# Optimization experiments

Hardware: AMD Instinct MI355X
Metric: run time of the kernel (lower is better)

Reference implementation:

```python
import jax, jax.numpy as jnp
import numpy as np

N_NODES = 50000
N_EDGES = 800000
D = 128


def setup_inputs() -> dict:
    key = jax.random.key(0)
    ks = jax.random.split(key, 6)
    stdv = 1.0 / np.sqrt(D)
    inputs = {
        "input": jax.random.normal(ks[0], (N_NODES, D), dtype=jnp.float32),
        "h0": jax.random.normal(ks[1], (N_NODES, D), dtype=jnp.float32),
        # COO representation of the (normalized) sparse adjacency
        "vals": jax.random.uniform(ks[2], (N_EDGES,), dtype=jnp.float32) / 16.0,
        "weight": jax.random.uniform(ks[3], (D, D), dtype=jnp.float32, minval=-stdv, maxval=stdv),
        "lamda": jnp.float32(0.5),
        "alpha": jnp.float32(0.1),
        "row": jax.random.randint(ks[4], (N_EDGES,), 0, N_NODES),
        "col": jax.random.randint(ks[5], (N_EDGES,), 0, N_NODES),
        "l": 4,
    }
    return inputs


def reference(input, h0, vals, weight, lamda, alpha, row, col, l):
    # theta = log(lamda / l + 1)
    theta = jnp.log(lamda / l + 1.0)
    # hi = spmm(adj, input): gather source-node features, scale by edge
    # values, scatter-add into destination rows.  [E, D] -> [N, D]
    hi = jax.ops.segment_sum(vals[:, None] * input[col], row, num_segments=input.shape[0])
    # variant=False path
    support = (1.0 - alpha) * hi + alpha * h0
    r = support
    # output = theta * support @ W + (1 - theta) * r
    output = theta * jnp.matmul(support, weight) + (1.0 - theta) * r
    return output
```

## Files before the change

kernel.cpp:

```cpp
#include <hip/hip_runtime.h>
#include <cmath>

constexpr int N_NODES = 50000;
constexpr int N_EDGES = 800000;
constexpr int D = 128;
constexpr int BM = 128;
constexpr int CAP = 32;
constexpr int OVF_CAP = 8192;

constexpr int NPART = 8;
constexpr int ROWS_PER_PART = (N_NODES + NPART - 1) / NPART;
constexpr int EPB = 8192;
constexpr int BPP = (N_EDGES + EPB - 1) / EPB;

constexpr int PRE_BLOCKS  = (N_EDGES / 4 + 255) / 256;
constexpr int CAST_BLOCKS = (N_NODES * D / 8 + 255) / 256;

constexpr size_t OFF_OVFCNT = 200000;
constexpr size_t OFF_BUCKET = 200064;
constexpr size_t OFF_OVF    = 6600064;
constexpr size_t OFF_PACKED = 6731136;
constexpr size_t OFF_ECV    = 19531136;
constexpr size_t OFF_ROW16  = 22731136;

__device__ __forceinline__ unsigned bf16rn(float f) {
    unsigned u = __float_as_uint(f);
    return (u + 0x7fffu + ((u >> 16) & 1u)) >> 16;
}
__device__ __forceinline__ float bf_lo(unsigned u) { return __uint_as_float(u << 16); }
__device__ __forceinline__ float bf_hi(unsigned u) { return __uint_as_float(u & 0xffff0000u); }

__device__ __forceinline__ unsigned enc_val(float v) {
    int m = (int)(v * 1048576.0f + 0.5f);
    if (m > 65535) m = 65535;
    if (m < 0) m = 0;
    return (unsigned)m;
}

__global__ __launch_bounds__(256) void prepack_cast(
    const int* __restrict__ row, const int* __restrict__ col,
    const float* __restrict__ vals, const float* __restrict__ input,
    ushort* __restrict__ row16, unsigned* __restrict__ ecv,
    unsigned* __restrict__ packed)
{
    if (blockIdx.x < PRE_BLOCKS) {
        int i = blockIdx.x * 256 + threadIdx.x;
        if (i >= N_EDGES / 4) return;
        int4   r4 = ((const int4*)row)[i];
        int4   c4 = ((const int4*)col)[i];
        float4 v4 = ((const float4*)vals)[i];
        ushort4 r16;
        r16.x = (unsigned short)r4.x; r16.y = (unsigned short)r4.y;
        r16.z = (unsigned short)r4.z; r16.w = (unsigned short)r4.w;
        uint4 e4;
        e4.x = (unsigned)c4.x | (enc_val(v4.x) << 16);
        e4.y = (unsigned)c4.y | (enc_val(v4.y) << 16);
        e4.z = (unsigned)c4.z | (enc_val(v4.z) << 16);
        e4.w = (unsigned)c4.w | (enc_val(v4.w) << 16);
        ((ushort4*)row16)[i] = r16;
        ((uint4*)ecv)[i] = e4;
    } else {
        int i = (blockIdx.x - PRE_BLOCKS) * 256 + threadIdx.x;
        if (i >= N_NODES * D / 8) return;
        const float4* f = (const float4*)(input + (size_t)i * 8);
        float4 a = f[0], b = f[1];
        uint4 o;
        o.x = bf16rn(a.x) | (bf16rn(a.y) << 16);
        o.y = bf16rn(a.z) | (bf16rn(a.w) << 16);
        o.z = bf16rn(b.x) | (bf16rn(b.y) << 16);
        o.w = bf16rn(b.z) | (bf16rn(b.w) << 16);
        ((uint4*)packed)[i] = o;
    }
}

__global__ __launch_bounds__(256) void part_scatter(
    const ushort* __restrict__ row16, const unsigned* __restrict__ ecv,
    int* __restrict__ cnt, unsigned* __restrict__ bucket,
    int* __restrict__ ovf_cnt, int4* __restrict__ ovf)
{
    const int p  = blockIdx.x & (NPART - 1);
    const int cb = blockIdx.x / NPART;
    const int lo = p * ROWS_PER_PART;
    const int hi = lo + ROWS_PER_PART;
    const int gbase = cb * (EPB / 4);

    #pragma unroll
    for (int it = 0; it < EPB / 4 / 256; ++it) {
        int gi = gbase + it * 256 + threadIdx.x;
        if (gi >= N_EDGES / 4) break;
        ushort4 r4 = ((const ushort4*)row16)[gi];
        int e = gi * 4;
        int r;
        r = r4.x;
        if (r >= lo && r < hi) {
            unsigned ent = ecv[e];
            int pos = atomicAdd(&cnt[r], 1);
            if (pos < CAP) bucket[(size_t)r * CAP + pos] = ent;
            else { int o = atomicAdd(ovf_cnt, 1);
                   if (o < OVF_CAP) ovf[o] = make_int4(r, (int)(ent & 0xffffu),
                       __float_as_int((float)(ent >> 16) * (1.0f / 1048576.0f)), 0); }
        }
        r = r4.y;
        if (r >= lo && r < hi) {
            unsigned ent = ecv[e + 1];
            int pos = atomicAdd(&cnt[r], 1);
            if (pos < CAP) bucket[(size_t)r * CAP + pos] = ent;
            else { int o = atomicAdd(ovf_cnt, 1);
                   if (o < OVF_CAP) ovf[o] = make_int4(r, (int)(ent & 0xffffu),
                       __float_as_int((float)(ent >> 16) * (1.0f / 1048576.0f)), 0); }
        }
        r = r4.z;
        if (r >= lo && r < hi) {
            unsigned ent = ecv[e + 2];
            int pos = atomicAdd(&cnt[r], 1);
            if (pos < CAP) bucket[(size_t)r * CAP + pos] = ent;
            else { int o = atomicAdd(ovf_cnt, 1);
                   if (o < OVF_CAP) ovf[o] = make_int4(r, (int)(ent & 0xffffu),
                       __float_as_int((float)(ent >> 16) * (1.0f / 1048576.0f)), 0); }
        }
        r = r4.w;
        if (r >= lo && r < hi) {
            unsigned ent = ecv[e + 3];
            int pos = atomicAdd(&cnt[r], 1);
            if (pos < CAP) bucket[(size_t)r * CAP + pos] = ent;
            else { int o = atomicAdd(ovf_cnt, 1);
                   if (o < OVF_CAP) ovf[o] = make_int4(r, (int)(ent & 0xffffu),
                       __float_as_int((float)(ent >> 16) * (1.0f / 1048576.0f)), 0); }
        }
    }
}

__global__ __launch_bounds__(256) void gather_support(
    const unsigned* __restrict__ packed,
    const float* __restrict__ h0,
    const float* __restrict__ alpha_p,
    const int* __restrict__ cnt,
    const unsigned* __restrict__ bucket,
    float* __restrict__ support)
{
    const float alpha = *alpha_p;
    const float oma = 1.0f - alpha;
    const int wv   = threadIdx.x >> 6;
    const int lane = threadIdx.x & 63;
    const int q    = lane & 15;
    const int half = lane >> 4;

    const int g = blockIdx.x * 4 + wv;
    if (g >= N_NODES) return;

    int n = cnt[g];
    if (n > CAP) n = CAP;
    const unsigned* b = bucket + (size_t)g * CAP;
    const uint4* pk = (const uint4*)packed;

    float acc[8] = {0.f, 0.f, 0.f, 0.f, 0.f, 0.f, 0.f, 0.f};
    int e = half;
    for (; e + 4 < n; e += 8) {
        unsigned m0 = b[e];
        unsigned m1 = b[e + 4];
        float v0 = (float)(m0 >> 16) * (1.0f / 1048576.0f);
        float v1 = (float)(m1 >> 16) * (1.0f / 1048576.0f);
        uint4 x0 = pk[(size_t)(m0 & 0xffffu) * 16 + q];
        uint4 x1 = pk[(size_t)(m1 & 0xffffu) * 16 + q];
        acc[0] += v0 * bf_lo(x0.x); acc[1] += v0 * bf_hi(x0.x);
        acc[2] += v0 * bf_lo(x0.y); acc[3] += v0 * bf_hi(x0.y);
        acc[4] += v0 * bf_lo(x0.z); acc[5] += v0 * bf_hi(x0.z);
        acc[6] += v0 * bf_lo(x0.w); acc[7] += v0 * bf_hi(x0.w);
        acc[0] += v1 * bf_lo(x1.x); acc[1] += v1 * bf_hi(x1.x);
        acc[2] += v1 * bf_lo(x1.y); acc[3] += v1 * bf_hi(x1.y);
        acc[4] += v1 * bf_lo(x1.z); acc[5] += v1 * bf_hi(x1.z);
        acc[6] += v1 * bf_lo(x1.w); acc[7] += v1 * bf_hi(x1.w);
    }
    if (e < n) {
        unsigned m = b[e];
        float v = (float)(m >> 16) * (1.0f / 1048576.0f);
        uint4 x = pk[(size_t)(m & 0xffffu) * 16 + q];
        acc[0] += v * bf_lo(x.x); acc[1] += v * bf_hi(x.x);
        acc[2] += v * bf_lo(x.y); acc[3] += v * bf_hi(x.y);
        acc[4] += v * bf_lo(x.z); acc[5] += v * bf_hi(x.z);
        acc[6] += v * bf_lo(x.w); acc[7] += v * bf_hi(x.w);
    }
    #pragma unroll
    for (int j = 0; j < 8; ++j) {
        acc[j] += __shfl_xor(acc[j], 16);
        acc[j] += __shfl_xor(acc[j], 32);
    }
    if (half == 0) {
        const float* hp = h0 + (size_t)g * D + q * 8;
        float4 ha = *(const float4*)(hp);
        float4 hb = *(const float4*)(hp + 4);
        float* sp = support + (size_t)g * D + q * 8;
        float4 sa, sb;
        sa.x = oma * acc[0] + alpha * ha.x;
        sa.y = oma * acc[1] + alpha * ha.y;
        sa.z = oma * acc[2] + alpha * ha.z;
        sa.w = oma * acc[3] + alpha * ha.w;
        sb.x = oma * acc[4] + alpha * hb.x;
        sb.y = oma * acc[5] + alpha * hb.y;
        sb.z = oma * acc[6] + alpha * hb.z;
        sb.w = oma * acc[7] + alpha * hb.w;
        *(float4*)(sp) = sa;
        *(float4*)(sp + 4) = sb;
    }
}

__global__ __launch_bounds__(256) void ovf_apply(
    const float* __restrict__ input,
    const float* __restrict__ alpha_p,
    const int* __restrict__ ovf_cnt,
    const int4* __restrict__ ovf,
    float* __restrict__ support)
{
    int n = *ovf_cnt;
    if (n > OVF_CAP) n = OVF_CAP;
    const float oma = 1.0f - *alpha_p;
    for (int i = blockIdx.x * 256 + threadIdx.x; i < n * 2; i += gridDim.x * 256) {
        int idx = i >> 1, part = i & 1;
        int4 m = ovf[idx];
        float v = oma * __int_as_float(m.z);
        const float* x = input + (size_t)m.y * D + part * 64;
        float* s = support + (size_t)m.x * D + part * 64;
        for (int k = 0; k < 64; ++k) atomicAdd(&s[k], v * x[k]);
    }
}

__global__ __launch_bounds__(512, 1) void gemm_inplace(
    const float* __restrict__ weight,
    const float* __restrict__ lamda_p,
    const int* __restrict__ l_p,
    float* __restrict__ data)
{
    __shared__ float sW[D * D];
    __shared__ float sS[BM * (D + 4)];

    const int tid = threadIdx.x;
    const float lamda = *lamda_p;
    const float theta = logf(lamda / (float)(*l_p) + 1.0f);
    const float omt = 1.0f - theta;

    {
        const float4* W4 = (const float4*)weight;
        float4* sW4 = (float4*)sW;
        #pragma unroll
        for (int i = 0; i < 8; ++i)
            sW4[tid + i * 512] = W4[tid + i * 512];
    }

    const int row0 = blockIdx.x * BM;
    #pragma unroll
    for (int ii = 0; ii < 8; ++ii) {
        int i = tid + ii * 512;
        int rr = i >> 5;
        int cc = (i & 31) << 2;
        int g = row0 + rr;
        float4 s = make_float4(0.f, 0.f, 0.f, 0.f);
        if (g < N_NODES) s = *(const float4*)(data + (size_t)g * D + cc);
        *(float4*)(sS + rr * (D + 4) + cc) = s;
    }
    __syncthreads();

    const int tx = tid & 31;
    const int ty = tid >> 5;
    const int jc = tx << 2;
    const int rbase = ty << 3;

    float acc[8][4] = {};
    for (int k = 0; k < D; k += 4) {
        float4 w0 = *(const float4*)(sW + (k + 0) * D + jc);
        float4 w1 = *(const float4*)(sW + (k + 1) * D + jc);
        float4 w2 = *(const float4*)(sW + (k + 2) * D + jc);
        float4 w3 = *(const float4*)(sW + (k + 3) * D + jc);
        #pragma unroll
        for (int i = 0; i < 8; ++i) {
            float4 s = *(const float4*)(sS + (rbase + i) * (D + 4) + k);
            acc[i][0] += s.x * w0.x + s.y * w1.x + s.z * w2.x + s.w * w3.x;
            acc[i][1] += s.x * w0.y + s.y * w1.y + s.z * w2.y + s.w * w3.y;
            acc[i][2] += s.x * w0.z + s.y * w1.z + s.z * w2.z + s.w * w3.z;
            acc[i][3] += s.x * w0.w + s.y * w1.w + s.z * w2.w + s.w * w3.w;
        }
    }

    #pragma unroll
    for (int i = 0; i < 8; ++i) {
        int g = row0 + rbase + i;
        if (g >= N_NODES) continue;
        float4 s = *(const float4*)(sS + (rbase + i) * (D + 4) + jc);
        float4 o;
        o.x = theta * acc[i][0] + omt * s.x;
        o.y = theta * acc[i][1] + omt * s.y;
        o.z = theta * acc[i][2] + omt * s.z;
        o.w = theta * acc[i][3] + omt * s.w;
        *(float4*)(data + (size_t)g * D + jc) = o;
    }
}

extern "C" void kernel_launch(void* const* d_in, const int* in_sizes, int n_in,
                              void* d_out, int out_size, void* d_ws, size_t ws_size,
                              hipStream_t stream) {
    const float* input  = (const float*)d_in[0];
    const float* h0     = (const float*)d_in[1];
    const float* vals   = (const float*)d_in[2];
    const float* weight = (const float*)d_in[3];
    const float* lamda  = (const float*)d_in[4];
    const float* alpha  = (const float*)d_in[5];
    const int*   row    = (const int*)d_in[6];
    const int*   col    = (const int*)d_in[7];
    const int*   l      = (const int*)d_in[8];
    float* out = (float*)d_out;

    char* ws = (char*)d_ws;
    int*      cnt     = (int*)ws;
    int*      ovf_cnt = (int*)(ws + OFF_OVFCNT);
    unsigned* bucket  = (unsigned*)(ws + OFF_BUCKET);
    int4*     ovf     = (int4*)(ws + OFF_OVF);
    unsigned* packed  = (unsigned*)(ws + OFF_PACKED);
    unsigned* ecv     = (unsigned*)(ws + OFF_ECV);
    ushort*   row16   = (ushort*)(ws + OFF_ROW16);

    hipMemsetAsync(ws, 0, OFF_BUCKET, stream);

    prepack_cast<<<PRE_BLOCKS + CAST_BLOCKS, 256, 0, stream>>>(
        row, col, vals, input, row16, ecv, packed);

    part_scatter<<<NPART * BPP, 256, 0, stream>>>(
        row16, ecv, cnt, bucket, ovf_cnt, ovf);

    int gatherb = (N_NODES + 3) / 4;
    gather_support<<<gatherb, 256, 0, stream>>>(packed, h0, alpha, cnt, bucket, out);

    ovf_apply<<<8, 256, 0, stream>>>(input, alpha, ovf_cnt, ovf, out);

    int gemmb = (N_NODES + BM - 1) / BM;
    gemm_inplace<<<gemmb, 512, 0, stream>>>(weight, lamda, l, out);
}
```

Measured before the change: 229.1 us.

## Replace FP32 FMA GEMM with bf16 MFMA GEMM using pre-transposed weight

The dense support@W stage moves from a scalar FP32 shared-memory GEMM to a 16x16x32 bf16 MFMA kernel. Support rows are cast to bf16 while being staged into LDS. An extra block in the prepack kernel converts and transposes the weight to bf16 once. The aim is to cut the ALU cost of the 50000x128x128 GEMM and raise occupancy with smaller 64-row tiles. In exchange, the matmul inputs lose precision to bf16 and the epilogue writes are column-strided per lane rather than float4-vectorized.

```diff
diff --git a/kernel.cpp b/kernel.cpp
--- a/kernel.cpp
+++ b/kernel.cpp
@@ -4,7 +4,6 @@
 constexpr int N_NODES = 50000;
 constexpr int N_EDGES = 800000;
 constexpr int D = 128;
-constexpr int BM = 128;
 constexpr int CAP = 32;
 constexpr int OVF_CAP = 8192;
 
@@ -22,6 +21,10 @@
 constexpr size_t OFF_PACKED = 6731136;
 constexpr size_t OFF_ECV    = 19531136;
 constexpr size_t OFF_ROW16  = 22731136;
+constexpr size_t OFF_WT     = 24331136;
+
+typedef __attribute__((ext_vector_type(8))) short bf16x8;
+typedef __attribute__((ext_vector_type(4))) float f32x4;
 
 __device__ __forceinline__ unsigned bf16rn(float f) {
     unsigned u = __float_as_uint(f);
@@ -40,8 +43,9 @@
 __global__ __launch_bounds__(256) void prepack_cast(
     const int* __restrict__ row, const int* __restrict__ col,
     const float* __restrict__ vals, const float* __restrict__ input,
+    const float* __restrict__ weight,
     ushort* __restrict__ row16, unsigned* __restrict__ ecv,
-    unsigned* __restrict__ packed)
+    unsigned* __restrict__ packed, ushort* __restrict__ wt)
 {
     if (blockIdx.x < PRE_BLOCKS) {
         int i = blockIdx.x * 256 + threadIdx.x;
@@ -59,7 +63,7 @@
         e4.w = (unsigned)c4.w | (enc_val(v4.w) << 16);
         ((ushort4*)row16)[i] = r16;
         ((uint4*)ecv)[i] = e4;
-    } else {
+    } else if (blockIdx.x < PRE_BLOCKS + CAST_BLOCKS) {
         int i = (blockIdx.x - PRE_BLOCKS) * 256 + threadIdx.x;
         if (i >= N_NODES * D / 8) return;
         const float4* f = (const float4*)(input + (size_t)i * 8);
@@ -70,6 +74,13 @@
         o.z = bf16rn(b.x) | (bf16rn(b.y) << 16);
         o.w = bf16rn(b.z) | (bf16rn(b.w) << 16);
         ((uint4*)packed)[i] = o;
+    } else {
+        #pragma unroll
+        for (int j = 0; j < 64; ++j) {
+            int idx = threadIdx.x + j * 256;
+            int k = idx >> 7, n = idx & 127;
+            wt[n * 128 + k] = (ushort)bf16rn(weight[idx]);
+        }
     }
 }
 
@@ -224,73 +235,74 @@
     }
 }
 
-__global__ __launch_bounds__(512, 1) void gemm_inplace(
-    const float* __restrict__ weight,
+__global__ __launch_bounds__(256) void gemm_mfma(
+    const ushort* __restrict__ wt,
     const float* __restrict__ lamda_p,
     const int* __restrict__ l_p,
     float* __restrict__ data)
 {
-    __shared__ float sW[D * D];
-    __shared__ float sS[BM * (D + 4)];
+    constexpr int SP = 136;
+    __shared__ ushort sA[64 * SP];
+    __shared__ ushort sB[128 * SP];
 
     const int tid = threadIdx.x;
     const float lamda = *lamda_p;
     const float theta = logf(lamda / (float)(*l_p) + 1.0f);
     const float omt = 1.0f - theta;
-
-    {
-        const float4* W4 = (const float4*)weight;
-        float4* sW4 = (float4*)sW;
-        #pragma unroll
-        for (int i = 0; i < 8; ++i)
-            sW4[tid + i * 512] = W4[tid + i * 512];
-    }
-
-    const int row0 = blockIdx.x * BM;
-    #pragma unroll
-    for (int ii = 0; ii < 8; ++ii) {
-        int i = tid + ii * 512;
-        int rr = i >> 5;
-        int cc = (i & 31) << 2;
+    const int row0 = blockIdx.x * 64;
+
+    #pragma unroll
+    for (int j = 0; j < 8; ++j) {
+        int idx = j * 256 + tid;
+        int n  = idx >> 4;
+        int k8 = (idx & 15) << 3;
+        *(uint4*)(&sB[n * SP + k8]) = ((const uint4*)wt)[idx];
+    }
+    #pragma unroll
+    for (int j = 0; j < 8; ++j) {
+        int idx = j * 256 + tid;
+        int rr = idx >> 5;
+        int c4 = (idx & 31) << 2;
         int g = row0 + rr;
         float4 s = make_float4(0.f, 0.f, 0.f, 0.f);
-        if (g < N_NODES) s = *(const float4*)(data + (size_t)g * D + cc);
-        *(float4*)(sS + rr * (D + 4) + cc) = s;
+        if (g < N_NODES) s = *(const float4*)(data + (size_t)g * D + c4);
+        uint2 pkv;
+        pkv.x = bf16rn(s.x) | (bf16rn(s.y) << 16);
+        pkv.y = bf16rn(s.z) | (bf16rn(s.w) << 16);
+        *(uint2*)(&sA[rr * SP + c4]) = pkv;
     }
     __syncthreads();
 
-    const int tx = tid & 31;
-    const int ty = tid >> 5;
-    const int jc = tx << 2;
-    const int rbase = ty << 3;
-
-    float acc[8][4] = {};
-    for (int k = 0; k < D; k += 4) {
-        float4 w0 = *(const float4*)(sW + (k + 0) * D + jc);
-        float4 w1 = *(const float4*)(sW + (k + 1) * D + jc);
-        float4 w2 = *(const float4*)(sW + (k + 2) * D + jc);
-        float4 w3 = *(const float4*)(sW + (k + 3) * D + jc);
+    const int wave = tid >> 6;
+    const int lane = tid & 63;
+    const int m    = lane & 15;
+    const int quad = lane >> 4;
+    const int arow = wave * 16 + m;
+
+    f32x4 acc[8] = {};
+    #pragma unroll
+    for (int kb = 0; kb < 4; ++kb) {
+        bf16x8 a = *(const bf16x8*)(&sA[arow * SP + kb * 32 + quad * 8]);
         #pragma unroll
-        for (int i = 0; i < 8; ++i) {
-            float4 s = *(const float4*)(sS + (rbase + i) * (D + 4) + k);
-            acc[i][0] += s.x * w0.x + s.y * w1.x + s.z * w2.x + s.w * w3.x;
-            acc[i][1] += s.x * w0.y + s.y * w1.y + s.z * w2.y + s.w * w3.y;
-            acc[i][2] += s.x * w0.z + s.y * w1.z + s.z * w2.z + s.w * w3.z;
-            acc[i][3] += s.x * w0.w + s.y * w1.w + s.z * w2.w + s.w * w3.w;
-        }
-    }
-
-    #pragma unroll
-    for (int i = 0; i < 8; ++i) {
-        int g = row0 + rbase + i;
-        if (g >= N_NODES) continue;
-        float4 s = *(const float4*)(sS + (rbase + i) * (D + 4) + jc);
-        float4 o;
-        o.x = theta * acc[i][0] + omt * s.x;
-        o.y = theta * acc[i][1] + omt * s.y;
-        o.z = theta * acc[i][2] + omt * s.z;
-        o.w = theta * acc[i][3] + omt * s.w;
-        *(float4*)(data + (size_t)g * D + jc) = o;
+        for (int nt = 0; nt < 8; ++nt) {
+            bf16x8 b = *(const bf16x8*)(&sB[(nt * 16 + m) * SP + kb * 32 + quad * 8]);
+            acc[nt] = __builtin_amdgcn_mfma_f32_16x16x32_bf16(a, b, acc[nt], 0, 0, 0);
+        }
+    }
+
+    const int gbase = row0 + wave * 16 + quad * 4;
+    #pragma unroll
+    for (int nt = 0; nt < 8; ++nt) {
+        int colb = nt * 16 + m;
+        #pragma unroll
+        for (int i = 0; i < 4; ++i) {
+            int g = gbase + i;
+            if (g < N_NODES) {
+                size_t off = (size_t)g * D + colb;
+                float s = data[off];
+                data[off] = theta * acc[nt][i] + omt * s;
+            }
+        }
     }
 }
 
@@ -316,11 +328,12 @@
     unsigned* packed  = (unsigned*)(ws + OFF_PACKED);
     unsigned* ecv     = (unsigned*)(ws + OFF_ECV);
     ushort*   row16   = (ushort*)(ws + OFF_ROW16);
+    ushort*   wt      = (ushort*)(ws + OFF_WT);
 
     hipMemsetAsync(ws, 0, OFF_BUCKET, stream);
 
-    prepack_cast<<<PRE_BLOCKS + CAST_BLOCKS, 256, 0, stream>>>(
-        row, col, vals, input, row16, ecv, packed);
+    prepack_cast<<<PRE_BLOCKS + CAST_BLOCKS + 1, 256, 0, stream>>>(
+        row, col, vals, input, weight, row16, ecv, packed, wt);
 
     part_scatter<<<NPART * BPP, 256, 0, stream>>>(
         row16, ecv, cnt, bucket, ovf_cnt, ovf);
@@ -330,6 +343,6 @@
 
     ovf_apply<<<8, 256, 0, stream>>>(input, alpha, ovf_cnt, ovf, out);
 
-    int gemmb = (N_NODES + BM - 1) / BM;
-    gemm_inplace<<<gemmb, 512, 0, stream>>>(weight, lamda, l, out);
-}
+    int gemmb = (N_NODES + 63) / 64;
+    gemm_mfma<<<gemmb, 256, 0, stream>>>(wt, lamda, l, out);
+}
```

New measurement: 223.1 us. -2.6%, faster.
